# Optimization experiments

Measured on AMD Instinct MI355X. Metric: run time of the kernel, lower is better.

The kernel has to match this reference:

```python
import jax, jax.numpy as jnp
import numpy as np

NUM_HEADS = 32


def setup_inputs() -> dict:
    key = jax.random.key(0)
    ks = jax.random.split(key, 6)
    B, S, D = 1, 2048, 4096
    hd = D // NUM_HEADS  # 128
    x = jax.random.normal(ks[0], (B, S, D), dtype=jnp.float32)
    # true rotary frequencies: freqs_cis = exp(i * t * theta^{-2j/hd})
    inv_freq = 1.0 / (10000.0 ** (jnp.arange(0, hd, 2, dtype=jnp.float32) / hd))  # [hd//2]
    angles = jnp.arange(S, dtype=jnp.float32)[:, None] * inv_freq[None, :]  # [S, hd//2]
    freqs_cos = jnp.cos(angles)
    freqs_sin = jnp.sin(angles)
    scale = 0.02
    wq = jax.random.normal(ks[1], (D, D), dtype=jnp.float32) * scale
    wk = jax.random.normal(ks[2], (D, D), dtype=jnp.float32) * scale
    wv = jax.random.normal(ks[3], (D, D), dtype=jnp.float32) * scale
    wo = jax.random.normal(ks[4], (D, D), dtype=jnp.float32) * scale
    return {"x": x, "freqs_cos": freqs_cos, "freqs_sin": freqs_sin,
            "wq": wq, "wk": wk, "wv": wv, "wo": wo}


def _apply_rope(t, cos, sin):
    # t: [B, S, H, hd]; cos/sin: [S, hd//2]
    B, S, H, hd = t.shape
    tr = t.reshape(B, S, H, hd // 2, 2)
    a, b = tr[..., 0], tr[..., 1]
    c = cos[None, :, None, :]
    s = sin[None, :, None, :]
    out_r = a * c - b * s
    out_i = a * s + b * c
    return jnp.stack([out_r, out_i], axis=-1).reshape(B, S, H, hd)


def reference(x, freqs_cos, freqs_sin, wq, wk, wv, wo):
    B, S, D = x.shape
    H = NUM_HEADS
    hd = D // H
    xq = (x @ wq).reshape(B, S, H, hd)
    xk = (x @ wk).reshape(B, S, H, hd)
    xv = (x @ wv).reshape(B, S, H, hd)
    xq = _apply_rope(xq, freqs_cos, freqs_sin)
    xk = _apply_rope(xk, freqs_cos, freqs_sin)
    # [B, H, S, hd]
    xq = xq.transpose(0, 2, 1, 3)
    xk = xk.transpose(0, 2, 1, 3)
    xv = xv.transpose(0, 2, 1, 3)
    scores = jnp.einsum('bhqd,bhkd->bhqk', xq, xk) / jnp.sqrt(jnp.float32(hd))
    scores = jax.nn.softmax(scores.astype(jnp.float32), axis=-1).astype(xq.dtype)
    out = jnp.einsum('bhqk,bhkd->bhqd', scores, xv)
    out = out.transpose(0, 2, 1, 3).reshape(B, S, D)
    return out @ wo
```

## Files before the change

### kernel.cpp

```cpp
#include <hip/hip_runtime.h>
#include <hip/hip_bf16.h>

typedef __hip_bfloat16 bf16;
typedef __attribute__((ext_vector_type(8))) short short8;
typedef __attribute__((ext_vector_type(4))) short short4v;
typedef __attribute__((ext_vector_type(4))) float f32x4;

#define MFMA16(a, b, c) __builtin_amdgcn_mfma_f32_16x16x32_bf16((a), (b), (c), 0, 0, 0)

static __device__ __forceinline__ void gload_lds16(const bf16* g, bf16* l) {
  __builtin_amdgcn_global_load_lds((const __attribute__((address_space(1))) unsigned int*)g,
                                   (__attribute__((address_space(3))) unsigned int*)l,
                                   16, 0, 0);
}

__global__ __launch_bounds__(256) void castx_kernel(const float* __restrict__ x,
                                                    bf16* __restrict__ xb, int n) {
  int i = (blockIdx.x * 256 + threadIdx.x) * 8;
  if (i >= n) return;
  float4 v0 = *(const float4*)(x + i);
  float4 v1 = *(const float4*)(x + i + 4);
  bf16 tmp[8];
  tmp[0] = __float2bfloat16(v0.x); tmp[1] = __float2bfloat16(v0.y);
  tmp[2] = __float2bfloat16(v0.z); tmp[3] = __float2bfloat16(v0.w);
  tmp[4] = __float2bfloat16(v1.x); tmp[5] = __float2bfloat16(v1.y);
  tmp[6] = __float2bfloat16(v1.z); tmp[7] = __float2bfloat16(v1.w);
  *(short8*)(xb + i) = *(short8*)tmp;
}

__global__ __launch_bounds__(256) void tw_kernel(const float* __restrict__ W,
                                                 bf16* __restrict__ WT) {
  __shared__ bf16 tile[64][65];
  int b = blockIdx.x;
  int tk = (b >> 6) * 64;
  int tn = (b & 63) * 64;
  int t = threadIdx.x;
  int c = t & 63, r0 = t >> 6;
#pragma unroll
  for (int i = 0; i < 16; ++i) {
    int r = i * 4 + r0;
    tile[c][r] = __float2bfloat16(W[(size_t)(tk + r) * 4096 + tn + c]);
  }
  __syncthreads();
#pragma unroll
  for (int i = 0; i < 16; ++i) {
    int r = i * 4 + r0;
    WT[(size_t)(tn + r) * 4096 + tk + c] = tile[r][c];
  }
}

template <int EPI>
__global__ __launch_bounds__(512) void gemm4(const bf16* __restrict__ A,
                                             const bf16* __restrict__ Bt,
                                             void* __restrict__ Cv,
                                             int M, int N, int K,
                                             const float* __restrict__ fcos,
                                             const float* __restrict__ fsin) {
  __shared__ bf16 LDS[3][384 * 64];
  const int NB = N >> 8;
  int g = blockIdx.x;
  int nwg = (M >> 7) * NB;
  int wid = (g & 7) * (nwg >> 3) + (g >> 3);
  int bm = wid / NB, bn = wid % NB;
  int t = threadIdx.x, lane = t & 63, w = t >> 6;
  int wm = w >> 2, wn = w & 3;
  int lr = lane & 15, lg = lane >> 4;
  int rsw = lr & 7;
  f32x4 acc[4][4] = {};

  const bf16* Ab = A + (size_t)bm * 128 * K;
  const bf16* Bb = Bt + (size_t)bn * 256 * K;
  int srow = t >> 3;
  int sg = (t & 7) ^ (srow & 7);
  int NK = K >> 6;

#define STA(buf, kt2, i)                                                        \
  gload_lds16(Ab + (size_t)((i) * 64 + srow) * K + (kt2) * 64 + sg * 8,         \
              LDS[buf] + ((i) * 512 + w * 64) * 8)
#define STB(buf, kt2, i)                                                        \
  gload_lds16(Bb + (size_t)((i) * 64 + srow) * K + (kt2) * 64 + sg * 8,         \
              LDS[buf] + 128 * 64 + ((i) * 512 + w * 64) * 8)
#define AFRAG(la, m, kc) \
  (*(const short8*)((la) + (wm * 64 + (m) * 16 + lr) * 64 + ((((kc) * 4 + lg) ^ rsw) << 3)))
#define BFRAG(lb, nf, kc) \
  (*(const short8*)((lb) + (wn * 64 + (nf) * 16 + lr) * 64 + ((((kc) * 4 + lg) ^ rsw) << 3)))

  STA(0, 0, 0); STA(0, 0, 1);
  STB(0, 0, 0); STB(0, 0, 1); STB(0, 0, 2); STB(0, 0, 3);
  STA(1, 1, 0); STA(1, 1, 1);
  STB(1, 1, 0); STB(1, 1, 1); STB(1, 1, 2); STB(1, 1, 3);
  asm volatile("s_waitcnt vmcnt(6)" ::: "memory");
  __builtin_amdgcn_s_barrier();

  int cur = 0;
  for (int kt = 0; kt < NK; ++kt) {
    const bf16* la = LDS[cur];
    const bf16* lb = la + 128 * 64;
    int nb2 = cur + 2; if (nb2 >= 3) nb2 -= 3;
    bool pf = (kt + 2) < NK;
    short8 a0[2][2], a1[2][2], b0[2][2], b1[2][2];

#pragma unroll
    for (int i = 0; i < 2; ++i)
#pragma unroll
      for (int kc = 0; kc < 2; ++kc) {
        a0[i][kc] = AFRAG(la, i, kc);
        b0[i][kc] = BFRAG(lb, i, kc);
      }
    if (pf) { STA(nb2, kt + 2, 0); STA(nb2, kt + 2, 1); }
    __builtin_amdgcn_s_barrier();
    __builtin_amdgcn_s_setprio(1);
#pragma unroll
    for (int i = 0; i < 2; ++i)
#pragma unroll
      for (int j = 0; j < 2; ++j)
#pragma unroll
        for (int kc = 0; kc < 2; ++kc)
          acc[i][j] = MFMA16(a0[i][kc], b0[j][kc], acc[i][j]);
    __builtin_amdgcn_s_setprio(0);
    __builtin_amdgcn_s_barrier();

#pragma unroll
    for (int j = 0; j < 2; ++j)
#pragma unroll
      for (int kc = 0; kc < 2; ++kc)
        b1[j][kc] = BFRAG(lb, 2 + j, kc);
    if (pf) { STB(nb2, kt + 2, 0); STB(nb2, kt + 2, 1); }
    __builtin_amdgcn_s_barrier();
    __builtin_amdgcn_s_setprio(1);
#pragma unroll
    for (int i = 0; i < 2; ++i)
#pragma unroll
      for (int j = 0; j < 2; ++j)
#pragma unroll
        for (int kc = 0; kc < 2; ++kc)
          acc[i][2 + j] = MFMA16(a0[i][kc], b1[j][kc], acc[i][2 + j]);
    __builtin_amdgcn_s_setprio(0);
    __builtin_amdgcn_s_barrier();

#pragma unroll
    for (int i = 0; i < 2; ++i)
#pragma unroll
      for (int kc = 0; kc < 2; ++kc)
        a1[i][kc] = AFRAG(la, 2 + i, kc);
    if (pf) { STB(nb2, kt + 2, 2); STB(nb2, kt + 2, 3); }
    __builtin_amdgcn_s_barrier();
    __builtin_amdgcn_s_setprio(1);
#pragma unroll
    for (int i = 0; i < 2; ++i)
#pragma unroll
      for (int j = 0; j < 2; ++j)
#pragma unroll
        for (int kc = 0; kc < 2; ++kc)
          acc[2 + i][j] = MFMA16(a1[i][kc], b0[j][kc], acc[2 + i][j]);
    __builtin_amdgcn_s_setprio(0);
    __builtin_amdgcn_s_barrier();

    __builtin_amdgcn_s_setprio(1);
#pragma unroll
    for (int i = 0; i < 2; ++i)
#pragma unroll
      for (int j = 0; j < 2; ++j)
#pragma unroll
        for (int kc = 0; kc < 2; ++kc)
          acc[2 + i][2 + j] = MFMA16(a1[i][kc], b1[j][kc], acc[2 + i][2 + j]);
    __builtin_amdgcn_s_setprio(0);
    if (pf)
      asm volatile("s_waitcnt vmcnt(6)" ::: "memory");
    else
      asm volatile("s_waitcnt vmcnt(0)" ::: "memory");
    __builtin_amdgcn_s_barrier();

    cur = (cur + 1 == 3) ? 0 : cur + 1;
  }
#undef STA
#undef STB
#undef AFRAG
#undef BFRAG

#pragma unroll
  for (int m = 0; m < 4; ++m)
#pragma unroll
    for (int nf = 0; nf < 4; ++nf) {
      int col = bn * 256 + wn * 64 + nf * 16 + lr;
      int row0 = bm * 128 + wm * 64 + m * 16 + lg * 4;
      if constexpr (EPI == 1 || EPI == 2) {
        const float qs = (EPI == 1) ? 0.08838834764831845f : 1.0f;
        int ip = (col >> 1) & 63;
        float sgn = (col & 1) ? 1.0f : -1.0f;
#pragma unroll
        for (int r = 0; r < 4; ++r) {
          int row = row0 + r;
          float mine = acc[m][nf][r];
          float oth = __shfl_xor(mine, 1);
          float cv = fcos[row * 64 + ip];
          float sv = fsin[row * 64 + ip];
          float v = (mine * cv + sgn * oth * sv) * qs;
          ((bf16*)Cv)[(size_t)row * N + col] = __float2bfloat16(v);
        }
      } else if constexpr (EPI == 3) {
        bf16 tmp[4];
#pragma unroll
        for (int r = 0; r < 4; ++r) tmp[r] = __float2bfloat16(acc[m][nf][r]);
        *(short4v*)((bf16*)Cv + (size_t)col * M + row0) = *(short4v*)tmp;
      } else {
#pragma unroll
        for (int r = 0; r < 4; ++r) {
          int row = row0 + r;
          ((float*)Cv)[(size_t)row * N + col] = acc[m][nf][r];
        }
      }
    }
}

__global__ __launch_bounds__(512, 2) void attn_fwd(const bf16* __restrict__ Q,
                                                   const bf16* __restrict__ K,
                                                   const bf16* __restrict__ Vt,
                                                   bf16* __restrict__ O) {
  __shared__ bf16 Kbuf[2][64 * 128];
  __shared__ bf16 Vbuf[2][128 * 64];
  __shared__ char Ps_all[8][2][2048];
  const int S = 2048, D = 4096, HD = 128, NT = 32;
  int g = blockIdx.y * 8 + blockIdx.x;
  int wid = (g & 7) * 32 + (g >> 3);
  int h = wid >> 3, qb = wid & 7;
  int tid = threadIdx.x, lane = tid & 63, w = tid >> 6;
  int lr = lane & 15, lg = lane >> 4;
  int q0 = qb * 256 + w * 32;
  int swz = (lr & 7) << 4;

  const bf16* Kh = K + h * HD;
  const bf16* Vh = Vt + (size_t)h * HD * S;

  short8 aq[2][4];
#pragma unroll
  for (int u = 0; u < 2; ++u)
#pragma unroll
    for (int c = 0; c < 4; ++c)
      aq[u][c] = *(const short8*)(Q + (size_t)(q0 + u * 16 + lr) * D + h * HD + c * 32 + lg * 8);

  int kr = lane >> 4, ksl = lane & 15;
  int vr = lane >> 3, vsl = lane & 7;

  f32x4 accO[2][8] = {};
  float lsum[2] = {0.f, 0.f};

#define STAGE(b, ttile)                                                            \
  do {                                                                             \
    int kv0_ = (ttile) * 64;                                                       \
    _Pragma("unroll") for (int ii = 0; ii < 2; ++ii) {                             \
      int row = w * 8 + ii * 4 + kr;                                               \
      gload_lds16(Kh + (size_t)(kv0_ + row) * D + ((ksl ^ (row & 7)) << 3),        \
                  &Kbuf[b][(w * 8 + ii * 4) * 128]);                               \
    }                                                                              \
    _Pragma("unroll") for (int ii = 0; ii < 2; ++ii) {                             \
      int row = w * 16 + ii * 8 + vr;                                              \
      gload_lds16(Vh + (size_t)row * S + kv0_ + ((vsl ^ (row & 7)) << 3),          \
                  &Vbuf[b][(w * 16 + ii * 8) * 64]);                               \
    }                                                                              \
  } while (0)

  int cur = 0;
  STAGE(0, 0);
  for (int tt = 0; tt < NT; ++tt) {
    if (tt + 1 < NT) {
      STAGE(cur ^ 1, tt + 1);
      asm volatile("s_waitcnt vmcnt(4)" ::: "memory");
    } else {
      asm volatile("s_waitcnt vmcnt(0)" ::: "memory");
    }
    __builtin_amdgcn_s_barrier();
    const bf16* Kb_ = Kbuf[cur];
    const bf16* Vb_ = Vbuf[cur];

    f32x4 sf[2][4] = {};
#pragma unroll
    for (int j = 0; j < 4; ++j)
#pragma unroll
      for (int c = 0; c < 4; ++c) {
        short8 kf = *(const short8*)(Kb_ + (j * 16 + lr) * 128 +
                                     (((c * 4 + lg) ^ (lr & 7)) << 3));
        sf[0][j] = MFMA16(kf, aq[0][c], sf[0][j]);
        sf[1][j] = MFMA16(kf, aq[1][c], sf[1][j]);
      }
#pragma unroll
    for (int u = 0; u < 2; ++u) {
      char* Ps = Ps_all[w][u];
#pragma unroll
      for (int j = 0; j < 4; ++j) {
        float p0 = __expf(sf[u][j][0]);
        float p1 = __expf(sf[u][j][1]);
        float p2 = __expf(sf[u][j][2]);
        float p3 = __expf(sf[u][j][3]);
        lsum[u] += (p0 + p1) + (p2 + p3);
        bf16 pk[4] = {__float2bfloat16(p0), __float2bfloat16(p1),
                      __float2bfloat16(p2), __float2bfloat16(p3)};
        *(short4v*)(Ps + lr * 128 + ((j * 32 + lg * 8) ^ swz)) = *(short4v*)pk;
      }
    }
#pragma unroll
    for (int t2 = 0; t2 < 2; ++t2) {
      short8 pa0 = *(const short8*)(Ps_all[w][0] + lr * 128 + ((t2 * 64 + lg * 16) ^ swz));
      short8 pa1 = *(const short8*)(Ps_all[w][1] + lr * 128 + ((t2 * 64 + lg * 16) ^ swz));
#pragma unroll
      for (int n = 0; n < 8; ++n) {
        short8 bv = *(const short8*)(Vb_ + (n * 16 + lr) * 64 +
                                     (((t2 * 4 + lg) ^ (lr & 7)) << 3));
        accO[0][n] = MFMA16(pa0, bv, accO[0][n]);
        accO[1][n] = MFMA16(pa1, bv, accO[1][n]);
      }
    }
    __builtin_amdgcn_s_barrier();
    cur ^= 1;
  }
#undef STAGE

#pragma unroll
  for (int u = 0; u < 2; ++u) {
    float ls = lsum[u];
    ls += __shfl_xor(ls, 16);
    ls += __shfl_xor(ls, 32);
    float rs[4];
#pragma unroll
    for (int r = 0; r < 4; ++r)
      rs[r] = 1.f / __shfl(ls, lg * 4 + r);
#pragma unroll
    for (int n = 0; n < 8; ++n)
#pragma unroll
      for (int r = 0; r < 4; ++r) {
        int row = q0 + u * 16 + lg * 4 + r;
        int col = h * HD + n * 16 + lr;
        O[(size_t)row * D + col] = __float2bfloat16(accO[u][n][r] * rs[r]);
      }
  }
}

extern "C" void kernel_launch(void* const* d_in, const int* in_sizes, int n_in,
                              void* d_out, int out_size, void* d_ws, size_t ws_size,
                              hipStream_t stream) {
  const float* x    = (const float*)d_in[0];
  const float* fcos = (const float*)d_in[1];
  const float* fsin = (const float*)d_in[2];
  const float* wq   = (const float*)d_in[3];
  const float* wk   = (const float*)d_in[4];
  const float* wv   = (const float*)d_in[5];
  const float* wo   = (const float*)d_in[6];
  float* out = (float*)d_out;

  const int S = 2048, D = 4096;
  const size_t MB = 1024 * 1024;
  char* ws = (char*)d_ws;
  bf16* xb = (bf16*)(ws);
  bf16* wT = (bf16*)(ws + 16 * MB);
  bf16* Qb = (bf16*)(ws + 48 * MB);
  bf16* Kb = (bf16*)(ws + 64 * MB);
  bf16* Vt = (bf16*)(ws + 80 * MB);
  bf16* AO = (bf16*)(ws);

  int n = S * D;
  castx_kernel<<<n / (256 * 8), 256, 0, stream>>>(x, xb, n);

  tw_kernel<<<4096, 256, 0, stream>>>(wq, wT);
  gemm4<1><<<256, 512, 0, stream>>>(xb, wT, Qb, S, D, D, fcos, fsin);
  tw_kernel<<<4096, 256, 0, stream>>>(wk, wT);
  gemm4<2><<<256, 512, 0, stream>>>(xb, wT, Kb, S, D, D, fcos, fsin);
  tw_kernel<<<4096, 256, 0, stream>>>(wv, wT);
  gemm4<3><<<256, 512, 0, stream>>>(xb, wT, Vt, S, D, D, nullptr, nullptr);

  attn_fwd<<<dim3(8, 32), 512, 0, stream>>>(Qb, Kb, Vt, AO);

  tw_kernel<<<4096, 256, 0, stream>>>(wo, wT);
  gemm4<4><<<256, 512, 0, stream>>>(AO, wT, out, S, D, D, nullptr, nullptr);
}
```

Baseline: 452.1 us.

## Fuse Q and K projections into one 256x256-tile GEMM with RoPE epilogue

The Q and K projection GEMMs become a single kernel over a concatenated transposed weight (N=8192), using larger 256x256 tiles with a BK=32 three-stage LDS pipeline and 8x4 MFMA accumulators per wave. The epilogue picks the Q or K output by column section and applies RoPE and the Q scale. This removes one launch and raises per-block arithmetic intensity, but adds register pressure (128 accumulator floats per thread), a smaller K-step with more barriers per tile, and a different workspace layout.

```diff
diff --git a/kernel.cpp b/kernel.cpp
--- a/kernel.cpp
+++ b/kernel.cpp
@@ -49,13 +49,136 @@
   }
 }
 
+__global__ __launch_bounds__(512) void gemmQK(const bf16* __restrict__ A,
+                                              const bf16* __restrict__ Bt,
+                                              bf16* __restrict__ Qb,
+                                              bf16* __restrict__ Kb,
+                                              const float* __restrict__ fcos,
+                                              const float* __restrict__ fsin) {
+  __shared__ bf16 LDS[3 * 16384];
+  const int K = 4096, NK = 128;
+  int g = blockIdx.x;
+  int wid = (g & 7) * 32 + (g >> 3);
+  int bm = wid >> 5, bn = wid & 31;
+  int t = threadIdx.x, lane = t & 63, w = t >> 6;
+  int wm = w >> 2, wn = w & 3;
+  int lr = lane & 15, lg = lane >> 4;
+  int rg = lg ^ ((lr >> 1) & 3);
+  f32x4 acc[8][4] = {};
+
+  const bf16* Ab = A + (size_t)bm * 256 * K;
+  const bf16* Bb = Bt + (size_t)bn * 256 * K;
+  int srow = t >> 2;
+  int sg = (t & 3) ^ ((t >> 3) & 3);
+
+#define STG(buf, kt2, mat, i)                                                     \
+  gload_lds16(((mat) ? Bb : Ab) + (size_t)((i) * 128 + srow) * K + (kt2) * 32 + sg * 8, \
+              LDS + (buf) * 16384 + (mat) * 8192 + (i) * 4096 + w * 512)
+#define AFR(la, mi) \
+  (*(const short8*)(LDS + (la) + (wm * 128 + (mi) * 16 + lr) * 32 + (rg << 3)))
+#define BFR(la, nf) \
+  (*(const short8*)(LDS + (la) + 8192 + (wn * 64 + (nf) * 16 + lr) * 32 + (rg << 3)))
+
+  STG(0, 0, 0, 0); STG(0, 0, 0, 1); STG(0, 0, 1, 0); STG(0, 0, 1, 1);
+  STG(1, 1, 0, 0); STG(1, 1, 0, 1); STG(1, 1, 1, 0); STG(1, 1, 1, 1);
+  asm volatile("s_waitcnt vmcnt(4)" ::: "memory");
+  __builtin_amdgcn_s_barrier();
+
+  int cur = 0;
+  for (int kt = 0; kt < NK; ++kt) {
+    int la = cur * 16384;
+    int stb = (cur + 2 >= 3) ? cur - 1 : cur + 2;
+    bool pf = (kt + 2) < NK;
+    short8 b[4], a0, a1;
+
+    b[0] = BFR(la, 0); b[1] = BFR(la, 1); b[2] = BFR(la, 2); b[3] = BFR(la, 3);
+    a0 = AFR(la, 0); a1 = AFR(la, 1);
+    if (pf) STG(stb, kt + 2, 0, 0);
+    __builtin_amdgcn_s_barrier();
+    __builtin_amdgcn_s_setprio(1);
+#pragma unroll
+    for (int nf = 0; nf < 4; ++nf) {
+      acc[0][nf] = MFMA16(a0, b[nf], acc[0][nf]);
+      acc[1][nf] = MFMA16(a1, b[nf], acc[1][nf]);
+    }
+    __builtin_amdgcn_s_setprio(0);
+    __builtin_amdgcn_s_barrier();
+
+    a0 = AFR(la, 2); a1 = AFR(la, 3);
+    if (pf) STG(stb, kt + 2, 0, 1);
+    __builtin_amdgcn_s_barrier();
+    __builtin_amdgcn_s_setprio(1);
+#pragma unroll
+    for (int nf = 0; nf < 4; ++nf) {
+      acc[2][nf] = MFMA16(a0, b[nf], acc[2][nf]);
+      acc[3][nf] = MFMA16(a1, b[nf], acc[3][nf]);
+    }
+    __builtin_amdgcn_s_setprio(0);
+    __builtin_amdgcn_s_barrier();
+
+    a0 = AFR(la, 4); a1 = AFR(la, 5);
+    if (pf) STG(stb, kt + 2, 1, 0);
+    __builtin_amdgcn_s_barrier();
+    __builtin_amdgcn_s_setprio(1);
+#pragma unroll
+    for (int nf = 0; nf < 4; ++nf) {
+      acc[4][nf] = MFMA16(a0, b[nf], acc[4][nf]);
+      acc[5][nf] = MFMA16(a1, b[nf], acc[5][nf]);
+    }
+    __builtin_amdgcn_s_setprio(0);
+    __builtin_amdgcn_s_barrier();
+
+    a0 = AFR(la, 6); a1 = AFR(la, 7);
+    if (pf) STG(stb, kt + 2, 1, 1);
+    __builtin_amdgcn_s_barrier();
+    __builtin_amdgcn_s_setprio(1);
+#pragma unroll
+    for (int nf = 0; nf < 4; ++nf) {
+      acc[6][nf] = MFMA16(a0, b[nf], acc[6][nf]);
+      acc[7][nf] = MFMA16(a1, b[nf], acc[7][nf]);
+    }
+    __builtin_amdgcn_s_setprio(0);
+    if (pf)
+      asm volatile("s_waitcnt vmcnt(4)" ::: "memory");
+    else
+      asm volatile("s_waitcnt vmcnt(0)" ::: "memory");
+    __builtin_amdgcn_s_barrier();
+
+    cur = (cur + 1 == 3) ? 0 : cur + 1;
+  }
+#undef STG
+#undef AFR
+#undef BFR
+
+  int sect = bn >> 4, bnl = bn & 15;
+  bf16* Cb = sect ? Kb : Qb;
+  const float qs = sect ? 1.0f : 0.08838834764831845f;
+#pragma unroll
+  for (int mi = 0; mi < 8; ++mi)
+#pragma unroll
+    for (int nf = 0; nf < 4; ++nf) {
+      int col = bnl * 256 + wn * 64 + nf * 16 + lr;
+      int row0 = bm * 256 + wm * 128 + mi * 16 + lg * 4;
+      int ip = (col >> 1) & 63;
+      float sgn = (col & 1) ? 1.0f : -1.0f;
+#pragma unroll
+      for (int r = 0; r < 4; ++r) {
+        int row = row0 + r;
+        float mine = acc[mi][nf][r];
+        float oth = __shfl_xor(mine, 1);
+        float cv = fcos[row * 64 + ip];
+        float sv = fsin[row * 64 + ip];
+        float v = (mine * cv + sgn * oth * sv) * qs;
+        Cb[(size_t)row * 4096 + col] = __float2bfloat16(v);
+      }
+    }
+}
+
 template <int EPI>
 __global__ __launch_bounds__(512) void gemm4(const bf16* __restrict__ A,
                                              const bf16* __restrict__ Bt,
                                              void* __restrict__ Cv,
-                                             int M, int N, int K,
-                                             const float* __restrict__ fcos,
-                                             const float* __restrict__ fsin) {
+                                             int M, int N, int K) {
   __shared__ bf16 LDS[3][384 * 64];
   const int NB = N >> 8;
   int g = blockIdx.x;
@@ -184,21 +307,7 @@
     for (int nf = 0; nf < 4; ++nf) {
       int col = bn * 256 + wn * 64 + nf * 16 + lr;
       int row0 = bm * 128 + wm * 64 + m * 16 + lg * 4;
-      if constexpr (EPI == 1 || EPI == 2) {
-        const float qs = (EPI == 1) ? 0.08838834764831845f : 1.0f;
-        int ip = (col >> 1) & 63;
-        float sgn = (col & 1) ? 1.0f : -1.0f;
-#pragma unroll
-        for (int r = 0; r < 4; ++r) {
-          int row = row0 + r;
-          float mine = acc[m][nf][r];
-          float oth = __shfl_xor(mine, 1);
-          float cv = fcos[row * 64 + ip];
-          float sv = fsin[row * 64 + ip];
-          float v = (mine * cv + sgn * oth * sv) * qs;
-          ((bf16*)Cv)[(size_t)row * N + col] = __float2bfloat16(v);
-        }
-      } else if constexpr (EPI == 3) {
+      if constexpr (EPI == 3) {
         bf16 tmp[4];
 #pragma unroll
         for (int r = 0; r < 4; ++r) tmp[r] = __float2bfloat16(acc[m][nf][r]);
@@ -350,25 +459,25 @@
   const int S = 2048, D = 4096;
   const size_t MB = 1024 * 1024;
   char* ws = (char*)d_ws;
-  bf16* xb = (bf16*)(ws);
-  bf16* wT = (bf16*)(ws + 16 * MB);
-  bf16* Qb = (bf16*)(ws + 48 * MB);
-  bf16* Kb = (bf16*)(ws + 64 * MB);
-  bf16* Vt = (bf16*)(ws + 80 * MB);
-  bf16* AO = (bf16*)(ws);
+  bf16* xb  = (bf16*)(ws);
+  bf16* wT2 = (bf16*)(ws + 16 * MB);
+  bf16* Vt  = (bf16*)(ws + 48 * MB);
+  bf16* Qb  = (bf16*)(ws + 80 * MB);
+  bf16* Kb  = (bf16*)(ws + 96 * MB);
+  bf16* AO  = (bf16*)(ws);
 
   int n = S * D;
   castx_kernel<<<n / (256 * 8), 256, 0, stream>>>(x, xb, n);
 
-  tw_kernel<<<4096, 256, 0, stream>>>(wq, wT);
-  gemm4<1><<<256, 512, 0, stream>>>(xb, wT, Qb, S, D, D, fcos, fsin);
-  tw_kernel<<<4096, 256, 0, stream>>>(wk, wT);
-  gemm4<2><<<256, 512, 0, stream>>>(xb, wT, Kb, S, D, D, fcos, fsin);
-  tw_kernel<<<4096, 256, 0, stream>>>(wv, wT);
-  gemm4<3><<<256, 512, 0, stream>>>(xb, wT, Vt, S, D, D, nullptr, nullptr);
+  tw_kernel<<<4096, 256, 0, stream>>>(wq, wT2);
+  tw_kernel<<<4096, 256, 0, stream>>>(wk, wT2 + (size_t)4096 * 4096);
+  gemmQK<<<256, 512, 0, stream>>>(xb, wT2, Qb, Kb, fcos, fsin);
+
+  tw_kernel<<<4096, 256, 0, stream>>>(wv, wT2);
+  gemm4<3><<<256, 512, 0, stream>>>(xb, wT2, Vt, S, D, D);
 
   attn_fwd<<<dim3(8, 32), 512, 0, stream>>>(Qb, Kb, Vt, AO);
 
-  tw_kernel<<<4096, 256, 0, stream>>>(wo, wT);
-  gemm4<4><<<256, 512, 0, stream>>>(AO, wT, out, S, D, D, nullptr, nullptr);
-}
+  tw_kernel<<<4096, 256, 0, stream>>>(wo, wT2);
+  gemm4<4><<<256, 512, 0, stream>>>(AO, wT2, out, S, D, D);
+}
```

Measured after the change: 428.3 us. 5.3% less time.

## Use 256x256 GEMM tiles, double-buffered half-K LDS, and fuse Q/K projections

Applied to the files above, without the earlier changes.

The GEMM block tile grows from 128x256 to 256x256, so each wave computes 128x64 with 32 accumulators. The LDS pipeline changes from a triple buffer of 64-wide K slices to a double buffer split into two 32-wide halves with a new swizzle. The Q and K projections become one GEMM with N=8192 whose epilogue routes each half to its own output. The aim is more data reuse per LDS load and fewer kernel launches. The cost is much higher register pressure, and the V and O GEMMs now launch only 128 blocks, fewer than the CU count, which may leave the GPU underoccupied.

```diff
diff --git a/kernel.cpp b/kernel.cpp
--- a/kernel.cpp
+++ b/kernel.cpp
@@ -50,164 +50,161 @@
 }
 
 template <int EPI>
-__global__ __launch_bounds__(512) void gemm4(const bf16* __restrict__ A,
+__global__ __launch_bounds__(512) void gemm8(const bf16* __restrict__ A,
                                              const bf16* __restrict__ Bt,
                                              void* __restrict__ Cv,
-                                             int M, int N, int K,
+                                             void* __restrict__ Cv2,
+                                             int M, int N,
                                              const float* __restrict__ fcos,
                                              const float* __restrict__ fsin) {
-  __shared__ bf16 LDS[3][384 * 64];
+  __shared__ bf16 LDS[2 * 32768];
+  const int K = 4096, NK = 64;
   const int NB = N >> 8;
   int g = blockIdx.x;
-  int nwg = (M >> 7) * NB;
+  int nwg = (M >> 8) * NB;
   int wid = (g & 7) * (nwg >> 3) + (g >> 3);
   int bm = wid / NB, bn = wid % NB;
   int t = threadIdx.x, lane = t & 63, w = t >> 6;
   int wm = w >> 2, wn = w & 3;
   int lr = lane & 15, lg = lane >> 4;
-  int rsw = lr & 7;
-  f32x4 acc[4][4] = {};
-
-  const bf16* Ab = A + (size_t)bm * 128 * K;
+  int rsw = (lr >> 1) & 3;
+  f32x4 acc[8][4] = {};
+
+  const bf16* Ab = A + (size_t)bm * 256 * K;
   const bf16* Bb = Bt + (size_t)bn * 256 * K;
-  int srow = t >> 3;
-  int sg = (t & 7) ^ (srow & 7);
-  int NK = K >> 6;
-
-#define STA(buf, kt2, i)                                                        \
-  gload_lds16(Ab + (size_t)((i) * 64 + srow) * K + (kt2) * 64 + sg * 8,         \
-              LDS[buf] + ((i) * 512 + w * 64) * 8)
-#define STB(buf, kt2, i)                                                        \
-  gload_lds16(Bb + (size_t)((i) * 64 + srow) * K + (kt2) * 64 + sg * 8,         \
-              LDS[buf] + 128 * 64 + ((i) * 512 + w * 64) * 8)
-#define AFRAG(la, m, kc) \
-  (*(const short8*)((la) + (wm * 64 + (m) * 16 + lr) * 64 + ((((kc) * 4 + lg) ^ rsw) << 3)))
-#define BFRAG(lb, nf, kc) \
-  (*(const short8*)((lb) + (wn * 64 + (nf) * 16 + lr) * 64 + ((((kc) * 4 + lg) ^ rsw) << 3)))
-
-  STA(0, 0, 0); STA(0, 0, 1);
-  STB(0, 0, 0); STB(0, 0, 1); STB(0, 0, 2); STB(0, 0, 3);
-  STA(1, 1, 0); STA(1, 1, 1);
-  STB(1, 1, 0); STB(1, 1, 1); STB(1, 1, 2); STB(1, 1, 3);
-  asm volatile("s_waitcnt vmcnt(6)" ::: "memory");
+  int sr4 = t >> 2;
+  int sg = (t & 3) ^ ((t >> 3) & 3);
+
+#define SA(nb, kt2, kh)                                                          \
+  do {                                                                           \
+    _Pragma("unroll") for (int j = 0; j < 2; ++j)                                \
+      gload_lds16(Ab + (size_t)(j * 128 + sr4) * K + (kt2) * 64 + (kh) * 32 + sg * 8, \
+                  LDS + (nb) + (kh) * 8192 + (j * 512 + t) * 8);                 \
+  } while (0)
+#define SB(nb, kt2, kh)                                                          \
+  do {                                                                           \
+    _Pragma("unroll") for (int j = 0; j < 2; ++j)                                \
+      gload_lds16(Bb + (size_t)(j * 128 + sr4) * K + (kt2) * 64 + (kh) * 32 + sg * 8, \
+                  LDS + (nb) + 16384 + (kh) * 8192 + (j * 512 + t) * 8);         \
+  } while (0)
+#define AFR(base, kc, mi) \
+  (*(const short8*)(LDS + (base) + (kc) * 8192 + (wm * 128 + (mi) * 16 + lr) * 32 + ((lg ^ rsw) << 3)))
+#define BFR(base, kc, nf) \
+  (*(const short8*)(LDS + (base) + 16384 + (kc) * 8192 + (wn * 64 + (nf) * 16 + lr) * 32 + ((lg ^ rsw) << 3)))
+
+  SA(0, 0, 0); SB(0, 0, 0); SA(0, 0, 1); SB(0, 0, 1);
+  asm volatile("s_waitcnt vmcnt(4)" ::: "memory");
   __builtin_amdgcn_s_barrier();
 
   int cur = 0;
   for (int kt = 0; kt < NK; ++kt) {
-    const bf16* la = LDS[cur];
-    const bf16* lb = la + 128 * 64;
-    int nb2 = cur + 2; if (nb2 >= 3) nb2 -= 3;
-    bool pf = (kt + 2) < NK;
-    short8 a0[2][2], a1[2][2], b0[2][2], b1[2][2];
-
-#pragma unroll
-    for (int i = 0; i < 2; ++i)
-#pragma unroll
-      for (int kc = 0; kc < 2; ++kc) {
-        a0[i][kc] = AFRAG(la, i, kc);
-        b0[i][kc] = BFRAG(lb, i, kc);
-      }
-    if (pf) { STA(nb2, kt + 2, 0); STA(nb2, kt + 2, 1); }
+    int base = cur * 32768;
+    int nbf = (cur ^ 1) * 32768;
+    bool pf = (kt + 1) < NK;
+    short8 a[4], b[4];
+
+#pragma unroll
+    for (int nf = 0; nf < 4; ++nf) b[nf] = BFR(base, 0, nf);
+#pragma unroll
+    for (int i = 0; i < 4; ++i) a[i] = AFR(base, 0, i);
+    if (pf) SA(nbf, kt + 1, 0);
     __builtin_amdgcn_s_barrier();
     __builtin_amdgcn_s_setprio(1);
 #pragma unroll
-    for (int i = 0; i < 2; ++i)
-#pragma unroll
-      for (int j = 0; j < 2; ++j)
-#pragma unroll
-        for (int kc = 0; kc < 2; ++kc)
-          acc[i][j] = MFMA16(a0[i][kc], b0[j][kc], acc[i][j]);
+    for (int i = 0; i < 4; ++i)
+#pragma unroll
+      for (int nf = 0; nf < 4; ++nf)
+        acc[i][nf] = MFMA16(a[i], b[nf], acc[i][nf]);
     __builtin_amdgcn_s_setprio(0);
     __builtin_amdgcn_s_barrier();
 
 #pragma unroll
-    for (int j = 0; j < 2; ++j)
-#pragma unroll
-      for (int kc = 0; kc < 2; ++kc)
-        b1[j][kc] = BFRAG(lb, 2 + j, kc);
-    if (pf) { STB(nb2, kt + 2, 0); STB(nb2, kt + 2, 1); }
+    for (int i = 0; i < 4; ++i) a[i] = AFR(base, 0, 4 + i);
+    if (pf) SB(nbf, kt + 1, 0);
     __builtin_amdgcn_s_barrier();
     __builtin_amdgcn_s_setprio(1);
 #pragma unroll
-    for (int i = 0; i < 2; ++i)
-#pragma unroll
-      for (int j = 0; j < 2; ++j)
-#pragma unroll
-        for (int kc = 0; kc < 2; ++kc)
-          acc[i][2 + j] = MFMA16(a0[i][kc], b1[j][kc], acc[i][2 + j]);
-    __builtin_amdgcn_s_setprio(0);
-    __builtin_amdgcn_s_barrier();
-
-#pragma unroll
-    for (int i = 0; i < 2; ++i)
-#pragma unroll
-      for (int kc = 0; kc < 2; ++kc)
-        a1[i][kc] = AFRAG(la, 2 + i, kc);
-    if (pf) { STB(nb2, kt + 2, 2); STB(nb2, kt + 2, 3); }
-    __builtin_amdgcn_s_barrier();
-    __builtin_amdgcn_s_setprio(1);
-#pragma unroll
-    for (int i = 0; i < 2; ++i)
-#pragma unroll
-      for (int j = 0; j < 2; ++j)
-#pragma unroll
-        for (int kc = 0; kc < 2; ++kc)
-          acc[2 + i][j] = MFMA16(a1[i][kc], b0[j][kc], acc[2 + i][j]);
-    __builtin_amdgcn_s_setprio(0);
-    __builtin_amdgcn_s_barrier();
-
-    __builtin_amdgcn_s_setprio(1);
-#pragma unroll
-    for (int i = 0; i < 2; ++i)
-#pragma unroll
-      for (int j = 0; j < 2; ++j)
-#pragma unroll
-        for (int kc = 0; kc < 2; ++kc)
-          acc[2 + i][2 + j] = MFMA16(a1[i][kc], b1[j][kc], acc[2 + i][2 + j]);
+    for (int i = 0; i < 4; ++i)
+#pragma unroll
+      for (int nf = 0; nf < 4; ++nf)
+        acc[4 + i][nf] = MFMA16(a[i], b[nf], acc[4 + i][nf]);
     __builtin_amdgcn_s_setprio(0);
     if (pf)
-      asm volatile("s_waitcnt vmcnt(6)" ::: "memory");
+      asm volatile("s_waitcnt vmcnt(4)" ::: "memory");
     else
       asm volatile("s_waitcnt vmcnt(0)" ::: "memory");
     __builtin_amdgcn_s_barrier();
 
-    cur = (cur + 1 == 3) ? 0 : cur + 1;
-  }
-#undef STA
-#undef STB
-#undef AFRAG
-#undef BFRAG
-
-#pragma unroll
-  for (int m = 0; m < 4; ++m)
+#pragma unroll
+    for (int nf = 0; nf < 4; ++nf) b[nf] = BFR(base, 1, nf);
+#pragma unroll
+    for (int i = 0; i < 4; ++i) a[i] = AFR(base, 1, i);
+    if (pf) SA(nbf, kt + 1, 1);
+    __builtin_amdgcn_s_barrier();
+    __builtin_amdgcn_s_setprio(1);
+#pragma unroll
+    for (int i = 0; i < 4; ++i)
+#pragma unroll
+      for (int nf = 0; nf < 4; ++nf)
+        acc[i][nf] = MFMA16(a[i], b[nf], acc[i][nf]);
+    __builtin_amdgcn_s_setprio(0);
+    __builtin_amdgcn_s_barrier();
+
+#pragma unroll
+    for (int i = 0; i < 4; ++i) a[i] = AFR(base, 1, 4 + i);
+    if (pf) SB(nbf, kt + 1, 1);
+    __builtin_amdgcn_s_barrier();
+    __builtin_amdgcn_s_setprio(1);
+#pragma unroll
+    for (int i = 0; i < 4; ++i)
+#pragma unroll
+      for (int nf = 0; nf < 4; ++nf)
+        acc[4 + i][nf] = MFMA16(a[i], b[nf], acc[4 + i][nf]);
+    __builtin_amdgcn_s_setprio(0);
+    asm volatile("s_waitcnt vmcnt(4)" ::: "memory");
+    __builtin_amdgcn_s_barrier();
+
+    cur ^= 1;
+  }
+#undef SA
+#undef SB
+#undef AFR
+#undef BFR
+
+#pragma unroll
+  for (int mi = 0; mi < 8; ++mi)
 #pragma unroll
     for (int nf = 0; nf < 4; ++nf) {
-      int col = bn * 256 + wn * 64 + nf * 16 + lr;
-      int row0 = bm * 128 + wm * 64 + m * 16 + lg * 4;
-      if constexpr (EPI == 1 || EPI == 2) {
-        const float qs = (EPI == 1) ? 0.08838834764831845f : 1.0f;
+      int row0 = bm * 256 + wm * 128 + mi * 16 + lg * 4;
+      if constexpr (EPI == 1) {
+        int sect = bn >> 4, bnl = bn & 15;
+        bf16* Cb = sect ? (bf16*)Cv2 : (bf16*)Cv;
+        const float qs = sect ? 1.0f : 0.08838834764831845f;
+        int col = bnl * 256 + wn * 64 + nf * 16 + lr;
         int ip = (col >> 1) & 63;
         float sgn = (col & 1) ? 1.0f : -1.0f;
 #pragma unroll
         for (int r = 0; r < 4; ++r) {
           int row = row0 + r;
-          float mine = acc[m][nf][r];
+          float mine = acc[mi][nf][r];
           float oth = __shfl_xor(mine, 1);
           float cv = fcos[row * 64 + ip];
           float sv = fsin[row * 64 + ip];
           float v = (mine * cv + sgn * oth * sv) * qs;
-          ((bf16*)Cv)[(size_t)row * N + col] = __float2bfloat16(v);
+          Cb[(size_t)row * 4096 + col] = __float2bfloat16(v);
         }
       } else if constexpr (EPI == 3) {
+        int col = bn * 256 + wn * 64 + nf * 16 + lr;
         bf16 tmp[4];
 #pragma unroll
-        for (int r = 0; r < 4; ++r) tmp[r] = __float2bfloat16(acc[m][nf][r]);
+        for (int r = 0; r < 4; ++r) tmp[r] = __float2bfloat16(acc[mi][nf][r]);
         *(short4v*)((bf16*)Cv + (size_t)col * M + row0) = *(short4v*)tmp;
       } else {
+        int col = bn * 256 + wn * 64 + nf * 16 + lr;
 #pragma unroll
         for (int r = 0; r < 4; ++r) {
           int row = row0 + r;
-          ((float*)Cv)[(size_t)row * N + col] = acc[m][nf][r];
+          ((float*)Cv)[(size_t)row * N + col] = acc[mi][nf][r];
         }
       }
     }
@@ -350,25 +347,25 @@
   const int S = 2048, D = 4096;
   const size_t MB = 1024 * 1024;
   char* ws = (char*)d_ws;
-  bf16* xb = (bf16*)(ws);
-  bf16* wT = (bf16*)(ws + 16 * MB);
-  bf16* Qb = (bf16*)(ws + 48 * MB);
-  bf16* Kb = (bf16*)(ws + 64 * MB);
-  bf16* Vt = (bf16*)(ws + 80 * MB);
-  bf16* AO = (bf16*)(ws);
+  bf16* xb  = (bf16*)(ws);
+  bf16* wT2 = (bf16*)(ws + 16 * MB);
+  bf16* Vt  = (bf16*)(ws + 48 * MB);
+  bf16* Qb  = (bf16*)(ws + 80 * MB);
+  bf16* Kb  = (bf16*)(ws + 96 * MB);
+  bf16* AO  = (bf16*)(ws);
 
   int n = S * D;
   castx_kernel<<<n / (256 * 8), 256, 0, stream>>>(x, xb, n);
 
-  tw_kernel<<<4096, 256, 0, stream>>>(wq, wT);
-  gemm4<1><<<256, 512, 0, stream>>>(xb, wT, Qb, S, D, D, fcos, fsin);
-  tw_kernel<<<4096, 256, 0, stream>>>(wk, wT);
-  gemm4<2><<<256, 512, 0, stream>>>(xb, wT, Kb, S, D, D, fcos, fsin);
-  tw_kernel<<<4096, 256, 0, stream>>>(wv, wT);
-  gemm4<3><<<256, 512, 0, stream>>>(xb, wT, Vt, S, D, D, nullptr, nullptr);
+  tw_kernel<<<4096, 256, 0, stream>>>(wq, wT2);
+  tw_kernel<<<4096, 256, 0, stream>>>(wk, wT2 + (size_t)4096 * 4096);
+  gemm8<1><<<256, 512, 0, stream>>>(xb, wT2, Qb, Kb, S, 8192, fcos, fsin);
+
+  tw_kernel<<<4096, 256, 0, stream>>>(wv, wT2);
+  gemm8<3><<<128, 512, 0, stream>>>(xb, wT2, Vt, nullptr, S, D, nullptr, nullptr);
 
   attn_fwd<<<dim3(8, 32), 512, 0, stream>>>(Qb, Kb, Vt, AO);
 
-  tw_kernel<<<4096, 256, 0, stream>>>(wo, wT);
-  gemm4<4><<<256, 512, 0, stream>>>(AO, wT, out, S, D, D, nullptr, nullptr);
-}
+  tw_kernel<<<4096, 256, 0, stream>>>(wo, wT2);
+  gemm8<4><<<128, 512, 0, stream>>>(AO, wT2, out, nullptr, S, D, nullptr, nullptr);
+}
```

After: 482.4 us. 1.07x slower.
